# Optimization experiments

Hardware: AMD Instinct MI355X
Metric: run time of the kernel (lower is better)

The kernel has to match this reference:

```python
import jax, jax.numpy as jnp
import numpy as np

LAMBDA_COORD = 5.0
LAMBDA_NOOBJ = 0.5
NUM_CLASSES = 80


def setup_inputs() -> dict:
    key = jax.random.key(0)
    k1, k2 = jax.random.split(key)
    B, G, C5, T = 64, 80, NUM_CLASSES + 5, 50
    predictions = jax.random.normal(k1, (B, G, G, C5), dtype=jnp.float32)
    t = jax.random.uniform(k2, (B, T, 5), dtype=jnp.float32)  # coords in [0,1)
    # col 0 holds the class id as a float (cast with .long() in the original)
    targets = t.at[..., 0].set(jnp.floor(t[..., 0] * NUM_CLASSES))
    return {"predictions": predictions, "targets": targets}


def reference(predictions, targets):
    B, G, _, C5 = predictions.shape
    T = targets.shape[1]
    nc = C5 - 5

    cls_id = targets[..., 0].astype(jnp.int32)              # (B,T)
    xg = targets[..., 1] * G
    yg = targets[..., 2] * G
    wg = targets[..., 3] * G
    hg = targets[..., 4] * G

    # obj/coord/class path clamps the cell index (int() truncation == floor for >=0)
    gx = jnp.clip(xg.astype(jnp.int32), 0, G - 1)           # (B,T)
    gy = jnp.clip(yg.astype(jnp.int32), 0, G - 1)
    bidx = jnp.broadcast_to(jnp.arange(B)[:, None], (B, T))
    pred = predictions[bidx, gy, gx]                         # (B,T,C5) gather of responsible cells

    sp = jax.nn.softplus
    # BCEWithLogits(z, 1) = softplus(-z), summed over all targets
    obj_loss = sp(-pred[..., 0]).sum()

    x_t = xg - gx.astype(xg.dtype)
    y_t = yg - gy.astype(yg.dtype)
    coord_loss = LAMBDA_COORD * (
        ((jax.nn.sigmoid(pred[..., 1]) - x_t) ** 2).sum()
        + ((jax.nn.sigmoid(pred[..., 2]) - y_t) ** 2).sum()
        + ((pred[..., 3] - wg) ** 2).sum()
        + ((pred[..., 4] - hg) ** 2).sum()
    )

    # BCEWithLogits(z, onehot) summed = sum softplus(z) - z * t
    z = pred[..., 5:]                                        # (B,T,nc)
    onehot = jax.nn.one_hot(cls_id, nc, dtype=z.dtype)
    class_loss = (sp(z) - z * onehot).sum()

    # noobj path uses the UNclamped truncated index (coords in [0,1) so identical here)
    tx = xg.astype(jnp.int32)
    ty = yg.astype(jnp.int32)
    occupied = jnp.zeros((B, G, G), dtype=bool).at[bidx, ty, tx].set(True)
    noobj_loss = LAMBDA_NOOBJ * jnp.where(
        occupied, jnp.float32(0.0), sp(predictions[..., 0])
    ).sum()

    Bf = jnp.float32(B)
    obj_loss = obj_loss / Bf
    noobj_loss = noobj_loss / Bf
    coord_loss = coord_loss / Bf
    class_loss = class_loss / Bf
    total = obj_loss + noobj_loss + coord_loss + class_loss
    return total, obj_loss, noobj_loss, coord_loss, class_loss
```

## Files before the change

kernel.cpp:

```cpp
#include <hip/hip_runtime.h>
#include <math.h>

#define GRID_SZ 80
#define NT      50
#define C5      85
#define BATCH   64
#define TPB     320
#define CELLS   (GRID_SZ*GRID_SZ)
#define CPB     640
#define BPI     10
#define NGATHER (BATCH*BPI)
#define NBLK    (NGATHER + BATCH)
#define NSLOT   (NBLK*4)
#define MAGIC   0x5A17C0DEu

__device__ __forceinline__ float sp(float x) {
    return fmaxf(x, 0.0f) + __logf(1.0f + __expf(-fabsf(x)));
}


__global__ __launch_bounds__(TPB) void fused_kernel(const float* __restrict__ pred,
                                                    const float* __restrict__ tgt,
                                                    unsigned long long* __restrict__ slots,
                                                    float* __restrict__ out) {
    const int tid  = threadIdx.x;
    const int lane = tid & 63;
    const int w    = tid >> 6;

    float obj = 0.f, coord = 0.f, cls = 0.f, nob = 0.f;

    if (blockIdx.x < NGATHER) {
        const int b   = blockIdx.x / BPI;
        const int blk = blockIdx.x % BPI;

        const size_t cellbase = (size_t)b * CELLS + blk * CPB;
        const float p0a = pred[(cellbase + tid)       * C5];
        const float p0b = pred[(cellbase + tid + TPB) * C5];

        {
            const int gt = blockIdx.x * 5 + w;
            const int tb = gt / NT, tt = gt - tb * NT;
            const float* tp = tgt + ((size_t)tb * NT + tt) * 5;
            const float t0 = tp[0], t1 = tp[1], t2 = tp[2], t3 = tp[3], t4 = tp[4];
            const int   cid = (int)t0;
            const float xg = t1 * GRID_SZ, yg = t2 * GRID_SZ;
            const float wg = t3 * GRID_SZ, hg = t4 * GRID_SZ;
            const int gx = min(max((int)xg, 0), GRID_SZ - 1);
            const int gy = min(max((int)yg, 0), GRID_SZ - 1);
            const float xt = xg - (float)gx;
            const float yt = yg - (float)gy;
            const float* pp = pred + (((size_t)tb * GRID_SZ + gy) * GRID_SZ + gx) * C5;

            {
                const float p = pp[lane];
                if (lane == 0)      obj = sp(-p);
                else if (lane == 1) { const float s = 1.f / (1.f + __expf(-p)); const float d = s - xt; coord = d * d; }
                else if (lane == 2) { const float s = 1.f / (1.f + __expf(-p)); const float d = s - yt; coord = d * d; }
                else if (lane == 3) { const float d = p - wg; coord = d * d; }
                else if (lane == 4) { const float d = p - hg; coord = d * d; }
                else                cls = sp(p) - ((lane - 5) == cid ? p : 0.f);
            }
            const int c2 = lane + 64;
            if (c2 < C5) {
                const float p = pp[c2];
                cls += sp(p) - ((c2 - 5) == cid ? p : 0.f);
            }
        }

        nob = sp(p0a) + sp(p0b);
    } else {
        const int img = blockIdx.x - NGATHER;
        if (w == 0) {
            const int t = lane;
            int cell = -1 - t;
            if (t < NT) {
                const float* tp = tgt + ((size_t)img * NT + t) * 5;
                const int tx = (int)(tp[1] * GRID_SZ);
                const int ty = (int)(tp[2] * GRID_SZ);
                cell = ty * GRID_SZ + tx;
            }
            bool first = (t < NT);
            #pragma unroll
            for (int u = 0; u < NT; ++u) {
                const int cu = __shfl(cell, u);
                first &= !((u < t) && (cu == cell));
            }
            if (first)
                nob = -sp(pred[((size_t)img * CELLS + cell) * C5]);
        }
    }

    #pragma unroll
    for (int off = 32; off; off >>= 1) {
        obj   += __shfl_xor(obj,   off);
        coord += __shfl_xor(coord, off);
        cls   += __shfl_xor(cls,   off);
        nob   += __shfl_xor(nob,   off);
    }
    __shared__ float s_red[5][4];
    if (lane == 0) { s_red[w][0] = obj; s_red[w][1] = coord; s_red[w][2] = cls; s_red[w][3] = nob; }
    __syncthreads();
    if (tid < 4) {
        const float v = s_red[0][tid] + s_red[1][tid] + s_red[2][tid]
                      + s_red[3][tid] + s_red[4][tid];
        const unsigned u = __float_as_uint(v);
        const unsigned long long pk =
            (unsigned long long)u | ((unsigned long long)(u ^ MAGIC) << 32);
        __hip_atomic_store(&slots[(size_t)blockIdx.x * 4 + tid], pk,
                           __ATOMIC_RELAXED, __HIP_MEMORY_SCOPE_AGENT);
    }

    if (blockIdx.x == 0) {
        const bool has9 = (tid < 256);
        unsigned long long v[9];
        bool ok;
        do {
            ok = true;
            #pragma unroll
            for (int j = 0; j < 8; ++j)
                v[j] = __hip_atomic_load(&slots[tid + j * TPB],
                                         __ATOMIC_RELAXED, __HIP_MEMORY_SCOPE_AGENT);
            if (has9)
                v[8] = __hip_atomic_load(&slots[tid + 8 * TPB],
                                         __ATOMIC_RELAXED, __HIP_MEMORY_SCOPE_AGENT);
            #pragma unroll
            for (int j = 0; j < 8; ++j)
                ok &= ((unsigned)(v[j] >> 32) == (((unsigned)v[j]) ^ MAGIC));
            if (has9)
                ok &= ((unsigned)(v[8] >> 32) == (((unsigned)v[8]) ^ MAGIC));
        } while (!ok);
        float acc = 0.f;
        #pragma unroll
        for (int j = 0; j < 8; ++j) acc += __uint_as_float((unsigned)v[j]);
        if (has9) acc += __uint_as_float((unsigned)v[8]);

        #pragma unroll
        for (int off = 4; off <= 32; off <<= 1) acc += __shfl_xor(acc, off);

        __shared__ float s_fin[5][4];
        if (lane < 4) s_fin[w][lane] = acc;
        __syncthreads();
        if (tid == 0) {
            float sums[4];
            #pragma unroll
            for (int c = 0; c < 4; ++c)
                sums[c] = s_fin[0][c] + s_fin[1][c] + s_fin[2][c]
                        + s_fin[3][c] + s_fin[4][c];
            const float invB   = 1.f / (float)BATCH;
            const float objT   = sums[0] * invB;
            const float coordT = 5.0f * sums[1] * invB;
            const float clsT   = sums[2] * invB;
            const float nobT   = 0.5f * sums[3] * invB;
            out[0] = objT + nobT + coordT + clsT;
            out[1] = objT;
            out[2] = nobT;
            out[3] = coordT;
            out[4] = clsT;
        }
    }
}

extern "C" void kernel_launch(void* const* d_in, const int* in_sizes, int n_in,
                              void* d_out, int out_size, void* d_ws, size_t ws_size,
                              hipStream_t stream) {
    const float* pred = (const float*)d_in[0];
    const float* tgt  = (const float*)d_in[1];
    unsigned long long* slots = (unsigned long long*)d_ws;
    float* out = (float*)d_out;

    fused_kernel<<<NBLK, TPB, 0, stream>>>(pred, tgt, slots, out);
}
```

Measured before the change: 15.51 us.

## Publish per-wave partials and move correction blocks to front of grid

Gather blocks now write per-wave partial sums straight to global slots, which removes the block-level shared-memory reduction and barrier. The 64 per-image correction blocks move to the start of the grid, so block 0, which does the final reduction, is scheduled early and has little work of its own. In exchange the finalizer must poll and sum far more slots, and a fallback kernel runs when the workspace is too small.

```diff
diff --git a/kernel.cpp b/kernel.cpp
--- a/kernel.cpp
+++ b/kernel.cpp
@@ -9,9 +9,12 @@
 #define CELLS   (GRID_SZ*GRID_SZ)
 #define CPB     640
 #define BPI     10
+#define NCOR    BATCH
 #define NGATHER (BATCH*BPI)
-#define NBLK    (NGATHER + BATCH)
-#define NSLOT   (NBLK*4)
+#define NBLK    (NCOR + NGATHER)
+#define NGW     (NGATHER*5)
+#define GSLOTS  (NGW*4)
+#define NSLOT   (GSLOTS + NCOR*4)
 #define MAGIC   0x5A17C0DEu
 
 __device__ __forceinline__ float sp(float x) {
@@ -27,16 +30,174 @@
     const int lane = tid & 63;
     const int w    = tid >> 6;
 
-    float obj = 0.f, coord = 0.f, cls = 0.f, nob = 0.f;
-
-    if (blockIdx.x < NGATHER) {
-        const int b   = blockIdx.x / BPI;
-        const int blk = blockIdx.x % BPI;
+    if (blockIdx.x >= NCOR) {
+        const int gb  = blockIdx.x - NCOR;
+        const int b   = gb / BPI;
+        const int blk = gb % BPI;
 
         const size_t cellbase = (size_t)b * CELLS + blk * CPB;
         const float p0a = pred[(cellbase + tid)       * C5];
         const float p0b = pred[(cellbase + tid + TPB) * C5];
 
+        float obj = 0.f, coord = 0.f, cls = 0.f;
+        {
+            const int gt = gb * 5 + w;
+            const int tb = gt / NT, tt = gt - tb * NT;
+            const float* tp = tgt + ((size_t)tb * NT + tt) * 5;
+            const float t0 = tp[0], t1 = tp[1], t2 = tp[2], t3 = tp[3], t4 = tp[4];
+            const int   cid = (int)t0;
+            const float xg = t1 * GRID_SZ, yg = t2 * GRID_SZ;
+            const float wg = t3 * GRID_SZ, hg = t4 * GRID_SZ;
+            const int gx = min(max((int)xg, 0), GRID_SZ - 1);
+            const int gy = min(max((int)yg, 0), GRID_SZ - 1);
+            const float xt = xg - (float)gx;
+            const float yt = yg - (float)gy;
+            const float* pp = pred + (((size_t)tb * GRID_SZ + gy) * GRID_SZ + gx) * C5;
+
+            {
+                const float p = pp[lane];
+                if (lane == 0)      obj = sp(-p);
+                else if (lane == 1) { const float s = 1.f / (1.f + __expf(-p)); const float d = s - xt; coord = d * d; }
+                else if (lane == 2) { const float s = 1.f / (1.f + __expf(-p)); const float d = s - yt; coord = d * d; }
+                else if (lane == 3) { const float d = p - wg; coord = d * d; }
+                else if (lane == 4) { const float d = p - hg; coord = d * d; }
+                else                cls = sp(p) - ((lane - 5) == cid ? p : 0.f);
+            }
+            const int c2 = lane + 64;
+            if (c2 < C5) {
+                const float p = pp[c2];
+                cls += sp(p) - ((c2 - 5) == cid ? p : 0.f);
+            }
+        }
+
+        float nob = sp(p0a) + sp(p0b);
+
+        #pragma unroll
+        for (int off = 32; off; off >>= 1) {
+            cls += __shfl_xor(cls, off);
+            nob += __shfl_xor(nob, off);
+        }
+        const float objS = __shfl(obj, 0);
+        float coordS = __shfl(coord, 1) + __shfl(coord, 2)
+                     + __shfl(coord, 3) + __shfl(coord, 4);
+
+        if (lane < 4) {
+            const float vals[4] = { objS, coordS, cls, nob };
+            const unsigned u = __float_as_uint(vals[lane]);
+            const unsigned long long pk =
+                (unsigned long long)u | ((unsigned long long)(u ^ MAGIC) << 32);
+            const int g = gb * 5 + w;
+            __hip_atomic_store(&slots[(size_t)g * 4 + lane], pk,
+                               __ATOMIC_RELAXED, __HIP_MEMORY_SCOPE_AGENT);
+        }
+        return;
+    }
+
+    const int img = blockIdx.x;
+    if (w == 0) {
+        const int t = lane;
+        int cell = -1 - t;
+        if (t < NT) {
+            const float* tp = tgt + ((size_t)img * NT + t) * 5;
+            const int tx = (int)(tp[1] * GRID_SZ);
+            const int ty = (int)(tp[2] * GRID_SZ);
+            cell = ty * GRID_SZ + tx;
+        }
+        bool first = (t < NT);
+        #pragma unroll
+        for (int u = 0; u < NT; ++u) {
+            const int cu = __shfl(cell, u);
+            first &= !((u < t) && (cu == cell));
+        }
+        float nob = 0.f;
+        if (first)
+            nob = -sp(pred[((size_t)img * CELLS + cell) * C5]);
+        #pragma unroll
+        for (int off = 32; off; off >>= 1) nob += __shfl_xor(nob, off);
+        if (lane < 4) {
+            const float v = (lane == 3) ? nob : 0.f;
+            const unsigned u = __float_as_uint(v);
+            const unsigned long long pk =
+                (unsigned long long)u | ((unsigned long long)(u ^ MAGIC) << 32);
+            __hip_atomic_store(&slots[(size_t)GSLOTS + img * 4 + lane], pk,
+                               __ATOMIC_RELAXED, __HIP_MEMORY_SCOPE_AGENT);
+        }
+    }
+
+    if (blockIdx.x == 0) {
+        float acc = 0.f;
+        #pragma unroll
+        for (int g = 0; g < 40; g += 8) {
+            unsigned long long v[8];
+            bool ok;
+            do {
+                ok = true;
+                #pragma unroll
+                for (int j = 0; j < 8; ++j)
+                    v[j] = __hip_atomic_load(&slots[tid + (g + j) * TPB],
+                                             __ATOMIC_RELAXED, __HIP_MEMORY_SCOPE_AGENT);
+                #pragma unroll
+                for (int j = 0; j < 8; ++j)
+                    ok &= ((unsigned)(v[j] >> 32) == (((unsigned)v[j]) ^ MAGIC));
+            } while (!ok);
+            #pragma unroll
+            for (int j = 0; j < 8; ++j) acc += __uint_as_float((unsigned)v[j]);
+        }
+        if (tid < NCOR * 4) {
+            unsigned long long v;
+            bool ok;
+            do {
+                v = __hip_atomic_load(&slots[GSLOTS + tid],
+                                      __ATOMIC_RELAXED, __HIP_MEMORY_SCOPE_AGENT);
+                ok = ((unsigned)(v >> 32) == (((unsigned)v) ^ MAGIC));
+            } while (!ok);
+            acc += __uint_as_float((unsigned)v);
+        }
+
+        #pragma unroll
+        for (int off = 4; off <= 32; off <<= 1) acc += __shfl_xor(acc, off);
+
+        __shared__ float s_fin[5][4];
+        if (lane < 4) s_fin[w][lane] = acc;
+        __syncthreads();
+        if (tid == 0) {
+            float sums[4];
+            #pragma unroll
+            for (int c = 0; c < 4; ++c)
+                sums[c] = s_fin[0][c] + s_fin[1][c] + s_fin[2][c]
+                        + s_fin[3][c] + s_fin[4][c];
+            const float invB   = 1.f / (float)BATCH;
+            const float objT   = sums[0] * invB;
+            const float coordT = 5.0f * sums[1] * invB;
+            const float clsT   = sums[2] * invB;
+            const float nobT   = 0.5f * sums[3] * invB;
+            out[0] = objT + nobT + coordT + clsT;
+            out[1] = objT;
+            out[2] = nobT;
+            out[3] = coordT;
+            out[4] = clsT;
+        }
+    }
+}
+
+#define FNGATHER 640
+#define FNBLK    (FNGATHER + BATCH)
+__global__ __launch_bounds__(TPB) void fused_fallback(const float* __restrict__ pred,
+                                                      const float* __restrict__ tgt,
+                                                      unsigned long long* __restrict__ slots,
+                                                      float* __restrict__ out) {
+    const int tid  = threadIdx.x;
+    const int lane = tid & 63;
+    const int w    = tid >> 6;
+
+    float obj = 0.f, coord = 0.f, cls = 0.f, nob = 0.f;
+
+    if (blockIdx.x < FNGATHER) {
+        const int b   = blockIdx.x / BPI;
+        const int blk = blockIdx.x % BPI;
+        const size_t cellbase = (size_t)b * CELLS + blk * CPB;
+        const float p0a = pred[(cellbase + tid)       * C5];
+        const float p0b = pred[(cellbase + tid + TPB) * C5];
         {
             const int gt = blockIdx.x * 5 + w;
             const int tb = gt / NT, tt = gt - tb * NT;
@@ -50,7 +211,6 @@
             const float xt = xg - (float)gx;
             const float yt = yg - (float)gy;
             const float* pp = pred + (((size_t)tb * GRID_SZ + gy) * GRID_SZ + gx) * C5;
-
             {
                 const float p = pp[lane];
                 if (lane == 0)      obj = sp(-p);
@@ -66,10 +226,9 @@
                 cls += sp(p) - ((c2 - 5) == cid ? p : 0.f);
             }
         }
-
         nob = sp(p0a) + sp(p0b);
     } else {
-        const int img = blockIdx.x - NGATHER;
+        const int img = blockIdx.x - FNGATHER;
         if (w == 0) {
             const int t = lane;
             int cell = -1 - t;
@@ -168,5 +327,8 @@
     unsigned long long* slots = (unsigned long long*)d_ws;
     float* out = (float*)d_out;
 
-    fused_kernel<<<NBLK, TPB, 0, stream>>>(pred, tgt, slots, out);
+    if (ws_size >= (size_t)NSLOT * 8)
+        fused_kernel<<<NBLK, TPB, 0, stream>>>(pred, tgt, slots, out);
+    else
+        fused_fallback<<<FNBLK, TPB, 0, stream>>>(pred, tgt, slots, out);
 }
```

Measured after the change: 16.36 us. 1.05x slower.
